# Kernel optimization log

Hardware: AMD Instinct MI355X
Metric: run time of the kernel (lower is better)

The kernel has to match this reference:

```python
import jax, jax.numpy as jnp
import numpy as np

B, N, EMB = 64, 2048, 128
K1 = 3
L = EMB - K1 + 1            # 126, width after conv1/conv2
K2 = L // 2 + 1             # 64, conv3 kernel width -> conv3 out width = K2 - 1 = 63


def _conv_relu(x, w, b):
    # x: [M, 1, H, W]; w: [O, 1, kh, kw]; VALID conv + bias + relu
    y = jax.lax.conv_general_dilated(
        x, w, window_strides=(1, 1), padding='VALID',
        dimension_numbers=('NCHW', 'OIHW', 'NCHW'))
    return jax.nn.relu(y + b[None, :, None, None])


def _score(pairs, W1, b1, W2, b2, W3, b3, fw1, fb1, fw2, fb2, fw3, fb3):
    # pairs: [M, 2, D] -> score [M]
    x = pairs[:, None]                                  # [M,1,2,D]
    c1 = _conv_relu(x, W1, b1)                          # [M,1,2,L]
    c2 = _conv_relu(x, W2, b2)                          # [M,1,1,L]
    c = jnp.concatenate([c1, c2], axis=2)               # [M,1,3,L]
    c3 = _conv_relu(c, W3, b3)                          # [M,1,1,K2-1]
    h = c3.reshape(c3.shape[0], -1)                     # [M,K2-1]
    h = h @ fw1.T + fb1                                 # [M,K2//4]
    h = h @ fw2.T + fb2                                 # [M,16]
    h = h @ fw3.T + fb3                                 # [M,1]
    return h[:, 0]


def setup_inputs() -> dict:
    key = jax.random.key(0)
    ks = jax.random.split(key, 12)
    users = jax.random.normal(ks[0], (B, N, EMB), jnp.float32)
    top_user = jax.random.normal(ks[1], (B, EMB), jnp.float32)
    question = jax.random.normal(ks[2], (B, EMB), jnp.float32)
    # ragged valid-lengths: uids nonzero for first `len` entries, zero after
    lengths = jax.random.randint(ks[3], (B,), 1, N + 1)
    vals = jax.random.randint(ks[4], (B, N), 1, 10000)
    uids = jnp.where(jnp.arange(N)[None, :] < lengths[:, None], vals, 0).astype(jnp.int64)
    s = 0.1
    return {
        'users': users, 'top_user': top_user, 'question': question, 'uids': uids,
        'W1': jax.random.normal(ks[5], (1, 1, 1, K1), jnp.float32) * s,
        'b1': jnp.zeros((1,), jnp.float32),
        'W2': jax.random.normal(ks[6], (1, 1, 2, K1), jnp.float32) * s,
        'b2': jnp.zeros((1,), jnp.float32),
        'W3': jax.random.normal(ks[7], (1, 1, 3, K2), jnp.float32) * s,
        'b3': jnp.zeros((1,), jnp.float32),
        'fw1': jax.random.normal(ks[8], (K2 // 4, K2 - 1), jnp.float32) * s,
        'fb1': jnp.zeros((K2 // 4,), jnp.float32),
        'fw2': jax.random.normal(ks[9], (16, K2 // 4), jnp.float32) * s,
        'fb2': jnp.zeros((16,), jnp.float32),
        'fw3': jax.random.normal(ks[10], (1, 16), jnp.float32) * s,
        'fb3': jnp.zeros((1,), jnp.float32),
    }


def reference(users, top_user, question, uids,
              W1, b1, W2, b2, W3, b3, fw1, fb1, fw2, fb2, fw3, fb3):
    b, n, d = users.shape
    params = (W1, b1, W2, b2, W3, b3, fw1, fb1, fw2, fb2, fw3, fb3)
    # low-rank pairs: (candidate user, question) for every candidate slot
    q = jnp.broadcast_to(question[:, None], (b, n, d))
    low = jnp.stack([users, q], axis=2).reshape(b * n, 2, d)      # [B*N,2,D]
    high = jnp.stack([top_user, question], axis=1)                # [B,2,D]
    low_s = _score(low, *params).reshape(b, n)                    # [B,N]
    high_s = _score(high, *params)                                # [B]
    # ragged length = index of first zero uid (torch loop breaks there)
    is_zero = uids == 0
    cnt = jnp.where(jnp.any(is_zero, axis=1), jnp.argmax(is_zero, axis=1), n)
    mask = (jnp.arange(n)[None, :] < cnt[:, None]).astype(low_s.dtype)
    return jnp.sum(jax.nn.sigmoid(low_s - high_s[:, None]) * mask)
```

## Files before the change

kernel.cpp:

```cpp
#include <hip/hip_runtime.h>
#include <hip/hip_bf16.h>

typedef __attribute__((ext_vector_type(8))) short short8v;
typedef __attribute__((ext_vector_type(4))) float float4v;

#define NB 64
#define NN 2048
#define ED 128
#define GRID_P 512

#define WS_WEFF  0
#define WS_BEFF  64
#define WS_SHIGH 128
#define WS_QTERM 192
#define WS_QPRE  (192+4096)
#define WS_BPACK (192+4096+8192)

static __device__ __forceinline__ unsigned int packbf2(float a, float b) {
    __hip_bfloat162 h = __float22bfloat162_rn(make_float2(a, b));
    return *(unsigned int*)&h;
}

__global__ __launch_bounds__(64) void k_prep(
    const float* __restrict__ top_user, const float* __restrict__ question,
    const float* __restrict__ W1, const float* __restrict__ b1,
    const float* __restrict__ W2, const float* __restrict__ b2,
    const float* __restrict__ W3, const float* __restrict__ b3,
    const float* __restrict__ fw1, const float* __restrict__ fb1,
    const float* __restrict__ fw2, const float* __restrict__ fb2,
    const float* __restrict__ fw3, const float* __restrict__ fb3,
    float* __restrict__ ws, float* __restrict__ out)
{
    const int lane = threadIdx.x;
    const int blk = blockIdx.x;
    __shared__ float g[16];
    __shared__ float w3s[192];
    w3s[lane] = W3[lane];
    w3s[64 + lane] = W3[64 + lane];
    w3s[128 + lane] = W3[128 + lane];
    if (lane < 16) {
        float s = 0.f;
        #pragma unroll
        for (int i = 0; i < 16; ++i) s += fw3[i] * fw2[i*16 + lane];
        g[lane] = s;
    }
    __syncthreads();

    if (blk >= NB) {
        const int kt = blk - NB;
        if (kt == 0) {
            if (lane == 0) out[0] = 0.f;
            float wv = 0.f;
            if (lane < 63) {
                #pragma unroll
                for (int k = 0; k < 16; ++k) wv += g[k] * fw1[k*63 + lane];
            }
            ws[WS_WEFF + lane] = wv;
            if (lane == 0) {
                float be = fb3[0];
                #pragma unroll
                for (int i = 0; i < 16; ++i) be += fw3[i] * fb2[i];
                #pragma unroll
                for (int k = 0; k < 16; ++k) be += g[k] * fb1[k];
                ws[WS_BEFF] = be;
            }
        }
        __hip_bfloat16* bp = (__hip_bfloat16*)(ws + WS_BPACK);
        const int g8 = (lane >> 4) * 8, li = lane & 15;
        #pragma unroll
        for (int nt = 0; nt < 4; ++nt) {
            const int tt = nt*16 + li;
            #pragma unroll
            for (int idx = 0; idx < 8; ++idx) {
                const int k = kt*32 + g8 + idx;
                const int j = k - tt;
                const int k2 = k - 128, j2 = k2 - tt;
                const bool v0 = (tt < 63) && (k < 126) && (j >= 0) && (j < 64);
                const bool v2 = (tt < 63) && (k2 >= 0) && (k2 < 126) && (j2 >= 0) && (j2 < 64);
                float v = (v0 ? w3s[j & 63] : 0.f) + (v2 ? w3s[128 + (j2 & 63)] : 0.f);
                bp[((kt*4 + nt)*64 + lane)*8 + idx] = __float2bfloat16(v);
            }
        }
        return;
    }

    float wv = 0.f;
    if (lane < 63) {
        #pragma unroll
        for (int k = 0; k < 16; ++k) wv += g[k] * fw1[k*63 + lane];
    }
    float be = fb3[0];
    #pragma unroll
    for (int i = 0; i < 16; ++i) be += fw3[i] * fb2[i];
    #pragma unroll
    for (int k = 0; k < 16; ++k) be += g[k] * fb1[k];

    __shared__ float q[132], tu[132], c1q[128], qt[64];
    __shared__ float4 D4[64];
    const int b = blk;
    ((float2*)q)[lane]  = ((const float2*)(question + b*ED))[lane];
    ((float2*)tu)[lane] = ((const float2*)(top_user + b*ED))[lane];
    if (lane == 63) {
        q[128]=0.f; q[129]=0.f; q[130]=0.f; q[131]=0.f;
        tu[128]=0.f; tu[129]=0.f; tu[130]=0.f; tu[131]=0.f;
    }
    __syncthreads();
    const float w10=W1[0], w11=W1[1], w12=W1[2];
    const float w20=W2[0], w21=W2[1], w22=W2[2];
    const float w23=W2[3], w24=W2[4], w25=W2[5];
    const float b1v=b1[0], b2v=b2[0], b3v=b3[0];
    const int i = 2*lane;
    float c1qa = fmaxf(b1v + w10*q[i]   + w11*q[i+1] + w12*q[i+2], 0.f);
    float c1qb = fmaxf(b1v + w10*q[i+1] + w11*q[i+2] + w12*q[i+3], 0.f);
    float qpa  = w23*q[i]   + w24*q[i+1] + w25*q[i+2];
    float qpb  = w23*q[i+1] + w24*q[i+2] + w25*q[i+3];
    float c1ta = fmaxf(b1v + w10*tu[i]   + w11*tu[i+1] + w12*tu[i+2], 0.f);
    float c1tb = fmaxf(b1v + w10*tu[i+1] + w11*tu[i+2] + w12*tu[i+3], 0.f);
    float c2a  = fmaxf(b2v + w20*tu[i]   + w21*tu[i+1] + w22*tu[i+2] + qpa, 0.f);
    float c2b  = fmaxf(b2v + w20*tu[i+1] + w21*tu[i+2] + w22*tu[i+3] + qpb, 0.f);
    if (lane == 63) { c1qa=0.f; c1qb=0.f; qpa=0.f; qpb=0.f; c1ta=0.f; c1tb=0.f; c2a=0.f; c2b=0.f; }
    c1q[i] = c1qa; c1q[i+1] = c1qb;
    ws[WS_QPRE + b*128 + i]     = qpa;
    ws[WS_QPRE + b*128 + i + 1] = qpb;
    D4[lane] = make_float4(c1ta, c2a, c1tb, c2b);
    __syncthreads();
    float qtv = 0.f;
    if (lane < 63) {
        #pragma unroll
        for (int j = 0; j < 64; ++j) qtv += w3s[64 + j] * c1q[lane + j];
    }
    qt[lane] = qtv;
    ws[WS_QTERM + b*64 + lane] = qtv + b3v;
    __syncthreads();
    float acc0 = b3v + qt[lane];
    float acc1 = 0.f;
    const float2* D2 = (const float2*)D4;
    #pragma unroll
    for (int j = 0; j < 64; ++j) {
        const float2 d = D2[lane + j];
        acc0 = fmaf(w3s[j],       d.x, acc0);
        acc1 = fmaf(w3s[128 + j], d.y, acc1);
    }
    float v = wv * fmaxf(acc0 + acc1, 0.f);
    #pragma unroll
    for (int off = 32; off > 0; off >>= 1) v += __shfl_xor(v, off, 64);
    if (lane == 0) ws[WS_SHIGH + b] = v + be;
}

__global__ __launch_bounds__(256) void k_pairs(
    const float* __restrict__ users, const int* __restrict__ uids,
    float* __restrict__ ws, float* __restrict__ out,
    const float* __restrict__ W1, const float* __restrict__ b1,
    const float* __restrict__ W2, const float* __restrict__ b2)
{
    __shared__ __align__(16) unsigned int X2[2][64][132];
    __shared__ float pscore[2][2][64];
    const int tid = threadIdx.x;
    const int w = tid >> 6, lane = tid & 63;
    const int bid = blockIdx.x;
    const int b = bid >> 3;
    const int cg = bid & 7;
    const int base = b*NN + cg*256;

    const int g = lane >> 4, li = lane & 15;
    const int nhalf = w >> 1;
    const int mbase = (w & 1) * 32;
    const int h = lane >> 5, j = lane & 31;
    const int r0 = w * 16;

    float4 bufA[8], bufB[8];
    #pragma unroll
    for (int pass = 0; pass < 8; ++pass) {
        const int r = r0 + pass*2 + h;
        bufA[pass] = *(const float4*)(users + (size_t)(base + r)*ED + 4*j);
    }
    const __hip_bfloat16* bp = (const __hip_bfloat16*)(ws + WS_BPACK);
    short8v bfr0[8], bfr1[8];
    #pragma unroll
    for (int kt = 0; kt < 8; ++kt) {
        bfr0[kt] = *(const short8v*)(bp + (((kt*4 + nhalf*2 + 0)*64 + lane) << 3));
        bfr1[kt] = *(const short8v*)(bp + (((kt*4 + nhalf*2 + 1)*64 + lane) << 3));
    }

    if (uids[base] == 0) return;
    const bool a1 = (uids[base +  64] != 0);
    const bool a2 = (uids[base + 128] != 0);
    const bool a3 = (uids[base + 192] != 0);

    const int m0 = (w == 0) ? uids[base + lane] : 1;
    const int m1 = (w == 0) ? uids[base +  64 + lane] : 1;
    const int m2 = (w == 0) ? uids[base + 128 + lane] : 1;
    const int m3 = (w == 0) ? uids[base + 192 + lane] : 1;

    #pragma unroll
    for (int pass = 0; pass < 8; ++pass) {
        const int r = r0 + pass*2 + h;
        bufB[pass] = *(const float4*)(users + (size_t)(base + 64 + r)*ED + 4*j);
    }

    const float w10=W1[0], w11=W1[1], w12=W1[2];
    const float w20=W2[0], w21=W2[1], w22=W2[2];
    const float b1v=b1[0], b2v=b2[0];

    const int t0 = nhalf*32 + li, t1 = t0 + 16;
    const float wf0 = ws[WS_WEFF + t0], wf1 = ws[WS_WEFF + t1];
    const float qt0 = ws[WS_QTERM + b*64 + t0], qt1 = ws[WS_QTERM + b*64 + t1];
    const float shigh = ws[WS_SHIGH + b], beff = ws[WS_BEFF];
    const float4 qp4 = *(const float4*)&ws[WS_QPRE + b*128 + 4*j];

#define PREP_BODY(BUF, XB)                                                          \
    {                                                                               \
        _Pragma("unroll")                                                           \
        for (int pass = 0; pass < 8; ++pass) {                                      \
            const int r = r0 + pass*2 + h;                                          \
            const float4 uu = BUF[pass];                                            \
            const float nx = __shfl(uu.x, (lane + 1) & 63, 64);                     \
            const float ny = __shfl(uu.y, (lane + 1) & 63, 64);                     \
            float c10 = fmaxf(b1v + w10*uu.x + w11*uu.y + w12*uu.z, 0.f);           \
            float c11 = fmaxf(b1v + w10*uu.y + w11*uu.z + w12*uu.w, 0.f);           \
            float c12 = fmaxf(b1v + w10*uu.z + w11*uu.w + w12*nx  , 0.f);           \
            float c13 = fmaxf(b1v + w10*uu.w + w11*nx   + w12*ny  , 0.f);           \
            float c20 = fmaxf(b2v + w20*uu.x + w21*uu.y + w22*uu.z + qp4.x, 0.f);   \
            float c21 = fmaxf(b2v + w20*uu.y + w21*uu.z + w22*uu.w + qp4.y, 0.f);   \
            float c22 = fmaxf(b2v + w20*uu.z + w21*uu.w + w22*nx   + qp4.z, 0.f);   \
            float c23 = fmaxf(b2v + w20*uu.w + w21*nx   + w22*ny   + qp4.w, 0.f);   \
            if (j == 31) { c12 = 0.f; c13 = 0.f; c22 = 0.f; c23 = 0.f; }            \
            uint2 v1; v1.x = packbf2(c10, c11); v1.y = packbf2(c12, c13);           \
            uint2 v2; v2.x = packbf2(c20, c21); v2.y = packbf2(c22, c23);           \
            *(uint2*)&X2[XB][r][2*j]      = v1;                                     \
            *(uint2*)&X2[XB][r][64 + 2*j] = v2;                                     \
        }                                                                           \
    }

    auto gemm = [&](int xb, int psl) {
        float4v acc00 = {0.f,0.f,0.f,0.f}, acc01 = {0.f,0.f,0.f,0.f};
        float4v acc10 = {0.f,0.f,0.f,0.f}, acc11 = {0.f,0.f,0.f,0.f};
        const char* Xb = (const char*)&X2[xb][0][0];
        #pragma unroll
        for (int kt = 0; kt < 8; ++kt) {
            const short8v aa0 = *(const short8v*)(Xb + (mbase + li)*528      + kt*64 + g*16);
            const short8v aa1 = *(const short8v*)(Xb + (mbase + 16 + li)*528 + kt*64 + g*16);
            acc00 = __builtin_amdgcn_mfma_f32_16x16x32_bf16(aa0, bfr0[kt], acc00, 0, 0, 0);
            acc01 = __builtin_amdgcn_mfma_f32_16x16x32_bf16(aa0, bfr1[kt], acc01, 0, 0, 0);
            acc10 = __builtin_amdgcn_mfma_f32_16x16x32_bf16(aa1, bfr0[kt], acc10, 0, 0, 0);
            acc11 = __builtin_amdgcn_mfma_f32_16x16x32_bf16(aa1, bfr1[kt], acc11, 0, 0, 0);
        }
        #pragma unroll
        for (int mi = 0; mi < 2; ++mi) {
            #pragma unroll
            for (int reg = 0; reg < 4; ++reg) {
                const float a0v = mi ? acc10[reg] : acc00[reg];
                const float a1v = mi ? acc11[reg] : acc01[reg];
                float v = wf0 * fmaxf(a0v + qt0, 0.f) + wf1 * fmaxf(a1v + qt1, 0.f);
                v += __shfl_xor(v, 1, 64);
                v += __shfl_xor(v, 2, 64);
                v += __shfl_xor(v, 4, 64);
                v += __shfl_xor(v, 8, 64);
                if (li == 0) pscore[psl][nhalf][mbase + mi*16 + g*4 + reg] = v;
            }
        }
    };

    float val = 0.f;
    auto sig = [&](int psl, int m) {
        if (w == 0) {
            const float d = pscore[psl][0][lane] + pscore[psl][1][lane] + beff - shigh;
            if (m != 0) val += 1.f / (1.f + __expf(-d));
        }
    };

    PREP_BODY(bufA, 0)
    __syncthreads();

    if (a2) {
        #pragma unroll
        for (int pass = 0; pass < 8; ++pass) {
            const int r = r0 + pass*2 + h;
            bufA[pass] = *(const float4*)(users + (size_t)(base + 128 + r)*ED + 4*j);
        }
    }
    gemm(0, 0);
    if (a1) PREP_BODY(bufB, 1)
    __syncthreads();

    sig(0, m0);
    if (a1) {
        if (a3) {
            #pragma unroll
            for (int pass = 0; pass < 8; ++pass) {
                const int r = r0 + pass*2 + h;
                bufB[pass] = *(const float4*)(users + (size_t)(base + 192 + r)*ED + 4*j);
            }
        }
        gemm(1, 1);
        if (a2) PREP_BODY(bufA, 0)
        __syncthreads();

        sig(1, m1);
        if (a2) {
            gemm(0, 0);
            if (a3) PREP_BODY(bufB, 1)
            __syncthreads();

            sig(0, m2);
            if (a3) {
                gemm(1, 1);
                __syncthreads();
                sig(1, m3);
            }
        }
    }

    if (w == 0) {
        #pragma unroll
        for (int off = 32; off > 0; off >>= 1) val += __shfl_xor(val, off, 64);
        if (lane == 0) atomicAdd(out, val);
    }
#undef PREP_BODY
}

extern "C" void kernel_launch(void* const* d_in, const int* in_sizes, int n_in,
                              void* d_out, int out_size, void* d_ws, size_t ws_size,
                              hipStream_t stream)
{
    const float* users    = (const float*)d_in[0];
    const float* top_user = (const float*)d_in[1];
    const float* question = (const float*)d_in[2];
    const int*   uids     = (const int*)d_in[3];
    const float* W1  = (const float*)d_in[4];
    const float* b1  = (const float*)d_in[5];
    const float* W2  = (const float*)d_in[6];
    const float* b2  = (const float*)d_in[7];
    const float* W3  = (const float*)d_in[8];
    const float* b3  = (const float*)d_in[9];
    const float* fw1 = (const float*)d_in[10];
    const float* fb1 = (const float*)d_in[11];
    const float* fw2 = (const float*)d_in[12];
    const float* fb2 = (const float*)d_in[13];
    const float* fw3 = (const float*)d_in[14];
    const float* fb3 = (const float*)d_in[15];
    float* ws  = (float*)d_ws;
    float* out = (float*)d_out;

    hipLaunchKernelGGL(k_prep, dim3(NB + 8), dim3(64), 0, stream,
                       top_user, question, W1, b1, W2, b2, W3, b3,
                       fw1, fb1, fw2, fb2, fw3, fb3, ws, out);
    hipLaunchKernelGGL(k_pairs, dim3(GRID_P), dim3(256), 0, stream,
                       users, uids, ws, out, W1, b1, W2, b2);
}
```

Before: 30.94 us.

## Restructure pair kernel into single-wave blocks of 64 rows without barriers

```diff
diff --git a/kernel.cpp b/kernel.cpp
--- a/kernel.cpp
+++ b/kernel.cpp
@@ -7,7 +7,7 @@
 #define NB 64
 #define NN 2048
 #define ED 128
-#define GRID_P 512
+#define GRID_P 2048
 
 #define WS_WEFF  0
 #define WS_BEFF  64
@@ -147,73 +147,66 @@
     if (lane == 0) ws[WS_SHIGH + b] = v + be;
 }
 
-__global__ __launch_bounds__(256) void k_pairs(
+__global__ __launch_bounds__(64, 2) void k_pairs(
     const float* __restrict__ users, const int* __restrict__ uids,
     float* __restrict__ ws, float* __restrict__ out,
     const float* __restrict__ W1, const float* __restrict__ b1,
     const float* __restrict__ W2, const float* __restrict__ b2)
 {
-    __shared__ __align__(16) unsigned int X2[2][64][132];
-    __shared__ float pscore[2][2][64];
-    const int tid = threadIdx.x;
-    const int w = tid >> 6, lane = tid & 63;
+    __shared__ __align__(16) unsigned int X[16][132];
+    const int lane = threadIdx.x;
     const int bid = blockIdx.x;
-    const int b = bid >> 3;
-    const int cg = bid & 7;
-    const int base = b*NN + cg*256;
+    const int b = bid >> 5;
+    const int cg = bid & 31;
+    const int base = b*NN + cg*64;
+
+    const int m_lane = uids[base + lane];
+    if (__shfl(m_lane, 0, 64) == 0) return;
+    const bool a1 = (__shfl(m_lane, 16, 64) != 0);
+    const bool a2 = (__shfl(m_lane, 32, 64) != 0);
+    const bool a3 = (__shfl(m_lane, 48, 64) != 0);
 
     const int g = lane >> 4, li = lane & 15;
-    const int nhalf = w >> 1;
-    const int mbase = (w & 1) * 32;
     const int h = lane >> 5, j = lane & 31;
-    const int r0 = w * 16;
-
-    float4 bufA[8], bufB[8];
+
+    float4 bufA[8];
     #pragma unroll
     for (int pass = 0; pass < 8; ++pass) {
-        const int r = r0 + pass*2 + h;
+        const int r = pass*2 + h;
         bufA[pass] = *(const float4*)(users + (size_t)(base + r)*ED + 4*j);
     }
+
     const __hip_bfloat16* bp = (const __hip_bfloat16*)(ws + WS_BPACK);
-    short8v bfr0[8], bfr1[8];
-    #pragma unroll
-    for (int kt = 0; kt < 8; ++kt) {
-        bfr0[kt] = *(const short8v*)(bp + (((kt*4 + nhalf*2 + 0)*64 + lane) << 3));
-        bfr1[kt] = *(const short8v*)(bp + (((kt*4 + nhalf*2 + 1)*64 + lane) << 3));
-    }
-
-    if (uids[base] == 0) return;
-    const bool a1 = (uids[base +  64] != 0);
-    const bool a2 = (uids[base + 128] != 0);
-    const bool a3 = (uids[base + 192] != 0);
-
-    const int m0 = (w == 0) ? uids[base + lane] : 1;
-    const int m1 = (w == 0) ? uids[base +  64 + lane] : 1;
-    const int m2 = (w == 0) ? uids[base + 128 + lane] : 1;
-    const int m3 = (w == 0) ? uids[base + 192 + lane] : 1;
-
-    #pragma unroll
-    for (int pass = 0; pass < 8; ++pass) {
-        const int r = r0 + pass*2 + h;
-        bufB[pass] = *(const float4*)(users + (size_t)(base + 64 + r)*ED + 4*j);
-    }
+    short8v bfr[32];
+    #pragma unroll
+    for (int nt = 0; nt < 4; ++nt) {
+        #pragma unroll
+        for (int kt = 0; kt < 8; ++kt) {
+            bfr[nt*8 + kt] = *(const short8v*)(bp + (((kt*4 + nt)*64 + lane) << 3));
+        }
+    }
+
+    float wfl[4], qtl[4];
+    #pragma unroll
+    for (int nt = 0; nt < 4; ++nt) {
+        wfl[nt] = ws[WS_WEFF + nt*16 + li];
+        qtl[nt] = ws[WS_QTERM + b*64 + nt*16 + li];
+    }
+    const float shigh = ws[WS_SHIGH + b], beff = ws[WS_BEFF];
+    const float4 qp4 = *(const float4*)&ws[WS_QPRE + b*128 + 4*j];
 
     const float w10=W1[0], w11=W1[1], w12=W1[2];
     const float w20=W2[0], w21=W2[1], w22=W2[2];
     const float b1v=b1[0], b2v=b2[0];
 
-    const int t0 = nhalf*32 + li, t1 = t0 + 16;
-    const float wf0 = ws[WS_WEFF + t0], wf1 = ws[WS_WEFF + t1];
-    const float qt0 = ws[WS_QTERM + b*64 + t0], qt1 = ws[WS_QTERM + b*64 + t1];
-    const float shigh = ws[WS_SHIGH + b], beff = ws[WS_BEFF];
-    const float4 qp4 = *(const float4*)&ws[WS_QPRE + b*128 + 4*j];
-
-#define PREP_BODY(BUF, XB)                                                          \
+    float val = 0.f;
+
+#define PREP_C()                                                                    \
     {                                                                               \
         _Pragma("unroll")                                                           \
         for (int pass = 0; pass < 8; ++pass) {                                      \
-            const int r = r0 + pass*2 + h;                                          \
-            const float4 uu = BUF[pass];                                            \
+            const int r = pass*2 + h;                                               \
+            const float4 uu = bufA[pass];                                           \
             const float nx = __shfl(uu.x, (lane + 1) & 63, 64);                     \
             const float ny = __shfl(uu.y, (lane + 1) & 63, 64);                     \
             float c10 = fmaxf(b1v + w10*uu.x + w11*uu.y + w12*uu.z, 0.f);           \
@@ -227,96 +220,76 @@
             if (j == 31) { c12 = 0.f; c13 = 0.f; c22 = 0.f; c23 = 0.f; }            \
             uint2 v1; v1.x = packbf2(c10, c11); v1.y = packbf2(c12, c13);           \
             uint2 v2; v2.x = packbf2(c20, c21); v2.y = packbf2(c22, c23);           \
-            *(uint2*)&X2[XB][r][2*j]      = v1;                                     \
-            *(uint2*)&X2[XB][r][64 + 2*j] = v2;                                     \
+            *(uint2*)&X[r][2*j]      = v1;                                          \
+            *(uint2*)&X[r][64 + 2*j] = v2;                                          \
         }                                                                           \
     }
 
-    auto gemm = [&](int xb, int psl) {
-        float4v acc00 = {0.f,0.f,0.f,0.f}, acc01 = {0.f,0.f,0.f,0.f};
-        float4v acc10 = {0.f,0.f,0.f,0.f}, acc11 = {0.f,0.f,0.f,0.f};
-        const char* Xb = (const char*)&X2[xb][0][0];
-        #pragma unroll
-        for (int kt = 0; kt < 8; ++kt) {
-            const short8v aa0 = *(const short8v*)(Xb + (mbase + li)*528      + kt*64 + g*16);
-            const short8v aa1 = *(const short8v*)(Xb + (mbase + 16 + li)*528 + kt*64 + g*16);
-            acc00 = __builtin_amdgcn_mfma_f32_16x16x32_bf16(aa0, bfr0[kt], acc00, 0, 0, 0);
-            acc01 = __builtin_amdgcn_mfma_f32_16x16x32_bf16(aa0, bfr1[kt], acc01, 0, 0, 0);
-            acc10 = __builtin_amdgcn_mfma_f32_16x16x32_bf16(aa1, bfr0[kt], acc10, 0, 0, 0);
-            acc11 = __builtin_amdgcn_mfma_f32_16x16x32_bf16(aa1, bfr1[kt], acc11, 0, 0, 0);
-        }
-        #pragma unroll
-        for (int mi = 0; mi < 2; ++mi) {
-            #pragma unroll
-            for (int reg = 0; reg < 4; ++reg) {
-                const float a0v = mi ? acc10[reg] : acc00[reg];
-                const float a1v = mi ? acc11[reg] : acc01[reg];
-                float v = wf0 * fmaxf(a0v + qt0, 0.f) + wf1 * fmaxf(a1v + qt1, 0.f);
-                v += __shfl_xor(v, 1, 64);
-                v += __shfl_xor(v, 2, 64);
-                v += __shfl_xor(v, 4, 64);
-                v += __shfl_xor(v, 8, 64);
-                if (li == 0) pscore[psl][nhalf][mbase + mi*16 + g*4 + reg] = v;
+#define LOAD_C(COFF)                                                                \
+    {                                                                               \
+        _Pragma("unroll")                                                           \
+        for (int pass = 0; pass < 8; ++pass) {                                      \
+            const int r = pass*2 + h;                                               \
+            bufA[pass] = *(const float4*)(users + (size_t)(base + (COFF) + r)*ED + 4*j); \
+        }                                                                           \
+    }
+
+#define GEMM_EP(COFF)                                                               \
+    {                                                                               \
+        float4v acc0 = {0.f,0.f,0.f,0.f}, acc1 = {0.f,0.f,0.f,0.f};                 \
+        float4v acc2 = {0.f,0.f,0.f,0.f}, acc3 = {0.f,0.f,0.f,0.f};                 \
+        const char* Xb = (const char*)&X[0][0];                                     \
+        _Pragma("unroll")                                                           \
+        for (int kt = 0; kt < 8; ++kt) {                                            \
+            const short8v a = *(const short8v*)(Xb + li*528 + kt*64 + g*16);        \
+            acc0 = __builtin_amdgcn_mfma_f32_16x16x32_bf16(a, bfr[0*8+kt], acc0, 0, 0, 0); \
+            acc1 = __builtin_amdgcn_mfma_f32_16x16x32_bf16(a, bfr[1*8+kt], acc1, 0, 0, 0); \
+            acc2 = __builtin_amdgcn_mfma_f32_16x16x32_bf16(a, bfr[2*8+kt], acc2, 0, 0, 0); \
+            acc3 = __builtin_amdgcn_mfma_f32_16x16x32_bf16(a, bfr[3*8+kt], acc3, 0, 0, 0); \
+        }                                                                           \
+        _Pragma("unroll")                                                           \
+        for (int reg = 0; reg < 4; ++reg) {                                         \
+            float v = wfl[0] * fmaxf(acc0[reg] + qtl[0], 0.f)                       \
+                    + wfl[1] * fmaxf(acc1[reg] + qtl[1], 0.f)                       \
+                    + wfl[2] * fmaxf(acc2[reg] + qtl[2], 0.f)                       \
+                    + wfl[3] * fmaxf(acc3[reg] + qtl[3], 0.f);                      \
+            v += __shfl_xor(v, 1, 64);                                              \
+            v += __shfl_xor(v, 2, 64);                                              \
+            v += __shfl_xor(v, 4, 64);                                              \
+            v += __shfl_xor(v, 8, 64);                                              \
+            const int mk = __shfl(m_lane, (COFF) + g*4 + reg, 64);                  \
+            if (li == 0 && mk != 0) {                                               \
+                const float d = v + beff - shigh;                                   \
+                val += 1.f / (1.f + __expf(-d));                                    \
+            }                                                                       \
+        }                                                                           \
+    }
+
+    PREP_C()
+    if (a1) LOAD_C(16)
+    GEMM_EP(0)
+    if (a1) {
+        PREP_C()
+        if (a2) LOAD_C(32)
+        GEMM_EP(16)
+        if (a2) {
+            PREP_C()
+            if (a3) LOAD_C(48)
+            GEMM_EP(32)
+            if (a3) {
+                PREP_C()
+                GEMM_EP(48)
             }
         }
-    };
-
-    float val = 0.f;
-    auto sig = [&](int psl, int m) {
-        if (w == 0) {
-            const float d = pscore[psl][0][lane] + pscore[psl][1][lane] + beff - shigh;
-            if (m != 0) val += 1.f / (1.f + __expf(-d));
-        }
-    };
-
-    PREP_BODY(bufA, 0)
-    __syncthreads();
-
-    if (a2) {
-        #pragma unroll
-        for (int pass = 0; pass < 8; ++pass) {
-            const int r = r0 + pass*2 + h;
-            bufA[pass] = *(const float4*)(users + (size_t)(base + 128 + r)*ED + 4*j);
-        }
-    }
-    gemm(0, 0);
-    if (a1) PREP_BODY(bufB, 1)
-    __syncthreads();
-
-    sig(0, m0);
-    if (a1) {
-        if (a3) {
-            #pragma unroll
-            for (int pass = 0; pass < 8; ++pass) {
-                const int r = r0 + pass*2 + h;
-                bufB[pass] = *(const float4*)(users + (size_t)(base + 192 + r)*ED + 4*j);
-            }
-        }
-        gemm(1, 1);
-        if (a2) PREP_BODY(bufA, 0)
-        __syncthreads();
-
-        sig(1, m1);
-        if (a2) {
-            gemm(0, 0);
-            if (a3) PREP_BODY(bufB, 1)
-            __syncthreads();
-
-            sig(0, m2);
-            if (a3) {
-                gemm(1, 1);
-                __syncthreads();
-                sig(1, m3);
-            }
-        }
-    }
-
-    if (w == 0) {
-        #pragma unroll
-        for (int off = 32; off > 0; off >>= 1) val += __shfl_xor(val, off, 64);
-        if (lane == 0) atomicAdd(out, val);
-    }
-#undef PREP_BODY
+    }
+
+    val += __shfl_xor(val, 16, 64);
+    val += __shfl_xor(val, 32, 64);
+    if (lane == 0) atomicAdd(out, val);
+
+#undef PREP_C
+#undef LOAD_C
+#undef GEMM_EP
 }
 
 extern "C" void kernel_launch(void* const* d_in, const int* in_sizes, int n_in,
@@ -345,6 +318,6 @@
     hipLaunchKernelGGL(k_prep, dim3(NB + 8), dim3(64), 0, stream,
                        top_user, question, W1, b1, W2, b2, W3, b3,
                        fw1, fb1, fw2, fb2, fw3, fb3, ws, out);
-    hipLaunchKernelGGL(k_pairs, dim3(GRID_P), dim3(256), 0, stream,
+    hipLaunchKernelGGL(k_pairs, dim3(GRID_P), dim3(64), 0, stream,
                        users, uids, ws, out, W1, b1, W2, b2);
 }
```

New measurement: 35.24 us. 1.14x slower.

## Compact active 64-row chunks into a work queue and load-balance across blocks

Applied to the files above, without the earlier changes.

```diff
diff --git a/kernel.cpp b/kernel.cpp
--- a/kernel.cpp
+++ b/kernel.cpp
@@ -15,6 +15,8 @@
 #define WS_QTERM 192
 #define WS_QPRE  (192+4096)
 #define WS_BPACK (192+4096+8192)
+#define WS_QCNT  (WS_BPACK+8192)
+#define WS_QLIST (WS_QCNT+8)
 
 static __device__ __forceinline__ unsigned int packbf2(float a, float b) {
     __hip_bfloat162 h = __float22bfloat162_rn(make_float2(a, b));
@@ -29,10 +31,30 @@
     const float* __restrict__ fw1, const float* __restrict__ fb1,
     const float* __restrict__ fw2, const float* __restrict__ fb2,
     const float* __restrict__ fw3, const float* __restrict__ fb3,
+    const int* __restrict__ uids,
     float* __restrict__ ws, float* __restrict__ out)
 {
     const int lane = threadIdx.x;
     const int blk = blockIdx.x;
+
+    if (blk >= NB + 8) {
+        const int s = blk - NB - 8;
+        int* qcnti  = (int*)(ws + WS_QCNT);
+        int* qlisti = (int*)(ws + WS_QLIST);
+        int running = 0;
+        #pragma unroll
+        for (int it = 0; it < 4; ++it) {
+            const int c = s*256 + it*64 + lane;
+            const int act = (uids[c * 64] != 0) ? 1 : 0;
+            const unsigned long long mask = __ballot(act);
+            const int pos = running + __popcll(mask & ((1ull << lane) - 1ull));
+            if (act) qlisti[s*256 + pos] = c;
+            running += (int)__popcll(mask);
+        }
+        if (lane == 0) qcnti[s] = running;
+        return;
+    }
+
     __shared__ float g[16];
     __shared__ float w3s[192];
     w3s[lane] = W3[lane];
@@ -158,22 +180,54 @@
     const int tid = threadIdx.x;
     const int w = tid >> 6, lane = tid & 63;
     const int bid = blockIdx.x;
-    const int b = bid >> 3;
-    const int cg = bid & 7;
-    const int base = b*NN + cg*256;
-
-    const int g = lane >> 4, li = lane & 15;
+
+    const int gfr = lane >> 4, li = lane & 15;
     const int nhalf = w >> 1;
     const int mbase = (w & 1) * 32;
     const int h = lane >> 5, j = lane & 31;
     const int r0 = w * 16;
 
+    const int* qcnti  = (const int*)(ws + WS_QCNT);
+    const int* qlisti = (const int*)(ws + WS_QLIST);
+    int pref[9]; pref[0] = 0;
+    #pragma unroll
+    for (int s = 0; s < 8; ++s) pref[s+1] = pref[s] + qcnti[s];
+    const int total = pref[8];
+    int myc[4];
+    #pragma unroll
+    for (int k = 0; k < 4; ++k) {
+        const int vid = bid + k*GRID_P;
+        int c = -1;
+        if (vid < total) {
+            int seg = 0;
+            #pragma unroll
+            for (int s = 1; s < 8; ++s) seg += (vid >= pref[s]) ? 1 : 0;
+            c = qlisti[seg*256 + (vid - pref[seg])];
+        }
+        myc[k] = c;
+    }
+    const int c0 = myc[0], c1 = myc[1], c2 = myc[2], c3 = myc[3];
+    if (c0 < 0) return;
+
+    const int pa0 = c0*64;
+    const int pa1 = (c1 >= 0) ? c1*64 : 0;
+    const int pa2 = (c2 >= 0) ? c2*64 : 0;
+    const int pa3 = (c3 >= 0) ? c3*64 : 0;
+
     float4 bufA[8], bufB[8];
     #pragma unroll
     for (int pass = 0; pass < 8; ++pass) {
         const int r = r0 + pass*2 + h;
-        bufA[pass] = *(const float4*)(users + (size_t)(base + r)*ED + 4*j);
-    }
+        bufA[pass] = *(const float4*)(users + (size_t)(pa0 + r)*ED + 4*j);
+    }
+    if (c1 >= 0) {
+        #pragma unroll
+        for (int pass = 0; pass < 8; ++pass) {
+            const int r = r0 + pass*2 + h;
+            bufB[pass] = *(const float4*)(users + (size_t)(pa1 + r)*ED + 4*j);
+        }
+    }
+
     const __hip_bfloat16* bp = (const __hip_bfloat16*)(ws + WS_BPACK);
     short8v bfr0[8], bfr1[8];
     #pragma unroll
@@ -182,33 +236,39 @@
         bfr1[kt] = *(const short8v*)(bp + (((kt*4 + nhalf*2 + 1)*64 + lane) << 3));
     }
 
-    if (uids[base] == 0) return;
-    const bool a1 = (uids[base +  64] != 0);
-    const bool a2 = (uids[base + 128] != 0);
-    const bool a3 = (uids[base + 192] != 0);
-
-    const int m0 = (w == 0) ? uids[base + lane] : 1;
-    const int m1 = (w == 0) ? uids[base +  64 + lane] : 1;
-    const int m2 = (w == 0) ? uids[base + 128 + lane] : 1;
-    const int m3 = (w == 0) ? uids[base + 192 + lane] : 1;
-
-    #pragma unroll
-    for (int pass = 0; pass < 8; ++pass) {
-        const int r = r0 + pass*2 + h;
-        bufB[pass] = *(const float4*)(users + (size_t)(base + 64 + r)*ED + 4*j);
-    }
+    const int t0 = nhalf*32 + li, t1 = t0 + 16;
+    const float wf0 = ws[WS_WEFF + t0], wf1 = ws[WS_WEFF + t1];
+    const float beff = ws[WS_BEFF];
+
+    const int b0 = c0 >> 5;
+    const float qta0 = ws[WS_QTERM + b0*64 + t0], qtb0 = ws[WS_QTERM + b0*64 + t1];
+    const float sh0 = ws[WS_SHIGH + b0];
+    const float4 qp0 = *(const float4*)&ws[WS_QPRE + b0*128 + 4*j];
+    const int m0 = (w == 0) ? uids[pa0 + lane] : 1;
+
+    const int b1i = (c1 >= 0) ? (c1 >> 5) : 0;
+    const float qta1 = ws[WS_QTERM + b1i*64 + t0], qtb1 = ws[WS_QTERM + b1i*64 + t1];
+    const float sh1 = ws[WS_SHIGH + b1i];
+    const float4 qp1 = *(const float4*)&ws[WS_QPRE + b1i*128 + 4*j];
+    const int m1 = (w == 0 && c1 >= 0) ? uids[pa1 + lane] : 1;
+
+    const int b2i = (c2 >= 0) ? (c2 >> 5) : 0;
+    const float qta2 = ws[WS_QTERM + b2i*64 + t0], qtb2 = ws[WS_QTERM + b2i*64 + t1];
+    const float sh2 = ws[WS_SHIGH + b2i];
+    const float4 qp2 = *(const float4*)&ws[WS_QPRE + b2i*128 + 4*j];
+    const int m2 = (w == 0 && c2 >= 0) ? uids[pa2 + lane] : 1;
+
+    const int b3i = (c3 >= 0) ? (c3 >> 5) : 0;
+    const float qta3 = ws[WS_QTERM + b3i*64 + t0], qtb3 = ws[WS_QTERM + b3i*64 + t1];
+    const float sh3 = ws[WS_SHIGH + b3i];
+    const float4 qp3 = *(const float4*)&ws[WS_QPRE + b3i*128 + 4*j];
+    const int m3 = (w == 0 && c3 >= 0) ? uids[pa3 + lane] : 1;
 
     const float w10=W1[0], w11=W1[1], w12=W1[2];
     const float w20=W2[0], w21=W2[1], w22=W2[2];
     const float b1v=b1[0], b2v=b2[0];
 
-    const int t0 = nhalf*32 + li, t1 = t0 + 16;
-    const float wf0 = ws[WS_WEFF + t0], wf1 = ws[WS_WEFF + t1];
-    const float qt0 = ws[WS_QTERM + b*64 + t0], qt1 = ws[WS_QTERM + b*64 + t1];
-    const float shigh = ws[WS_SHIGH + b], beff = ws[WS_BEFF];
-    const float4 qp4 = *(const float4*)&ws[WS_QPRE + b*128 + 4*j];
-
-#define PREP_BODY(BUF, XB)                                                          \
+#define PREP_BODY(BUF, XB, QP)                                                      \
     {                                                                               \
         _Pragma("unroll")                                                           \
         for (int pass = 0; pass < 8; ++pass) {                                      \
@@ -220,10 +280,10 @@
             float c11 = fmaxf(b1v + w10*uu.y + w11*uu.z + w12*uu.w, 0.f);           \
             float c12 = fmaxf(b1v + w10*uu.z + w11*uu.w + w12*nx  , 0.f);           \
             float c13 = fmaxf(b1v + w10*uu.w + w11*nx   + w12*ny  , 0.f);           \
-            float c20 = fmaxf(b2v + w20*uu.x + w21*uu.y + w22*uu.z + qp4.x, 0.f);   \
-            float c21 = fmaxf(b2v + w20*uu.y + w21*uu.z + w22*uu.w + qp4.y, 0.f);   \
-            float c22 = fmaxf(b2v + w20*uu.z + w21*uu.w + w22*nx   + qp4.z, 0.f);   \
-            float c23 = fmaxf(b2v + w20*uu.w + w21*nx   + w22*ny   + qp4.w, 0.f);   \
+            float c20 = fmaxf(b2v + w20*uu.x + w21*uu.y + w22*uu.z + QP.x, 0.f);    \
+            float c21 = fmaxf(b2v + w20*uu.y + w21*uu.z + w22*uu.w + QP.y, 0.f);    \
+            float c22 = fmaxf(b2v + w20*uu.z + w21*uu.w + w22*nx   + QP.z, 0.f);    \
+            float c23 = fmaxf(b2v + w20*uu.w + w21*nx   + w22*ny   + QP.w, 0.f);    \
             if (j == 31) { c12 = 0.f; c13 = 0.f; c22 = 0.f; c23 = 0.f; }            \
             uint2 v1; v1.x = packbf2(c10, c11); v1.y = packbf2(c12, c13);           \
             uint2 v2; v2.x = packbf2(c20, c21); v2.y = packbf2(c22, c23);           \
@@ -232,14 +292,23 @@
         }                                                                           \
     }
 
-    auto gemm = [&](int xb, int psl) {
+#define LOAD_INTO(BUF, PA)                                                          \
+    {                                                                               \
+        _Pragma("unroll")                                                           \
+        for (int pass = 0; pass < 8; ++pass) {                                      \
+            const int r = r0 + pass*2 + h;                                          \
+            BUF[pass] = *(const float4*)(users + (size_t)((PA) + r)*ED + 4*j);      \
+        }                                                                           \
+    }
+
+    auto gemm = [&](int xb, int psl, float qta, float qtb) {
         float4v acc00 = {0.f,0.f,0.f,0.f}, acc01 = {0.f,0.f,0.f,0.f};
         float4v acc10 = {0.f,0.f,0.f,0.f}, acc11 = {0.f,0.f,0.f,0.f};
         const char* Xb = (const char*)&X2[xb][0][0];
         #pragma unroll
         for (int kt = 0; kt < 8; ++kt) {
-            const short8v aa0 = *(const short8v*)(Xb + (mbase + li)*528      + kt*64 + g*16);
-            const short8v aa1 = *(const short8v*)(Xb + (mbase + 16 + li)*528 + kt*64 + g*16);
+            const short8v aa0 = *(const short8v*)(Xb + (mbase + li)*528      + kt*64 + gfr*16);
+            const short8v aa1 = *(const short8v*)(Xb + (mbase + 16 + li)*528 + kt*64 + gfr*16);
             acc00 = __builtin_amdgcn_mfma_f32_16x16x32_bf16(aa0, bfr0[kt], acc00, 0, 0, 0);
             acc01 = __builtin_amdgcn_mfma_f32_16x16x32_bf16(aa0, bfr1[kt], acc01, 0, 0, 0);
             acc10 = __builtin_amdgcn_mfma_f32_16x16x32_bf16(aa1, bfr0[kt], acc10, 0, 0, 0);
@@ -251,62 +320,50 @@
             for (int reg = 0; reg < 4; ++reg) {
                 const float a0v = mi ? acc10[reg] : acc00[reg];
                 const float a1v = mi ? acc11[reg] : acc01[reg];
-                float v = wf0 * fmaxf(a0v + qt0, 0.f) + wf1 * fmaxf(a1v + qt1, 0.f);
+                float v = wf0 * fmaxf(a0v + qta, 0.f) + wf1 * fmaxf(a1v + qtb, 0.f);
                 v += __shfl_xor(v, 1, 64);
                 v += __shfl_xor(v, 2, 64);
                 v += __shfl_xor(v, 4, 64);
                 v += __shfl_xor(v, 8, 64);
-                if (li == 0) pscore[psl][nhalf][mbase + mi*16 + g*4 + reg] = v;
+                if (li == 0) pscore[psl][nhalf][mbase + mi*16 + gfr*4 + reg] = v;
             }
         }
     };
 
     float val = 0.f;
-    auto sig = [&](int psl, int m) {
+    auto sig = [&](int psl, int m, float sh) {
         if (w == 0) {
-            const float d = pscore[psl][0][lane] + pscore[psl][1][lane] + beff - shigh;
+            const float d = pscore[psl][0][lane] + pscore[psl][1][lane] + beff - sh;
             if (m != 0) val += 1.f / (1.f + __expf(-d));
         }
     };
 
-    PREP_BODY(bufA, 0)
-    __syncthreads();
-
-    if (a2) {
-        #pragma unroll
-        for (int pass = 0; pass < 8; ++pass) {
-            const int r = r0 + pass*2 + h;
-            bufA[pass] = *(const float4*)(users + (size_t)(base + 128 + r)*ED + 4*j);
-        }
-    }
-    gemm(0, 0);
-    if (a1) PREP_BODY(bufB, 1)
-    __syncthreads();
-
-    sig(0, m0);
-    if (a1) {
-        if (a3) {
-            #pragma unroll
-            for (int pass = 0; pass < 8; ++pass) {
-                const int r = r0 + pass*2 + h;
-                bufB[pass] = *(const float4*)(users + (size_t)(base + 192 + r)*ED + 4*j);
-            }
-        }
-        gemm(1, 1);
-        if (a2) PREP_BODY(bufA, 0)
+    PREP_BODY(bufA, 0, qp0)
+    __syncthreads();
+
+    if (c2 >= 0) LOAD_INTO(bufA, pa2)
+    gemm(0, 0, qta0, qtb0);
+    if (c1 >= 0) PREP_BODY(bufB, 1, qp1)
+    __syncthreads();
+
+    sig(0, m0, sh0);
+    if (c1 >= 0) {
+        if (c3 >= 0) LOAD_INTO(bufB, pa3)
+        gemm(1, 1, qta1, qtb1);
+        if (c2 >= 0) PREP_BODY(bufA, 0, qp2)
         __syncthreads();
 
-        sig(1, m1);
-        if (a2) {
-            gemm(0, 0);
-            if (a3) PREP_BODY(bufB, 1)
+        sig(1, m1, sh1);
+        if (c2 >= 0) {
+            gemm(0, 0, qta2, qtb2);
+            if (c3 >= 0) PREP_BODY(bufB, 1, qp3)
             __syncthreads();
 
-            sig(0, m2);
-            if (a3) {
-                gemm(1, 1);
+            sig(0, m2, sh2);
+            if (c3 >= 0) {
+                gemm(1, 1, qta3, qtb3);
                 __syncthreads();
-                sig(1, m3);
+                sig(1, m3, sh3);
             }
         }
     }
@@ -317,6 +374,7 @@
         if (lane == 0) atomicAdd(out, val);
     }
 #undef PREP_BODY
+#undef LOAD_INTO
 }
 
 extern "C" void kernel_launch(void* const* d_in, const int* in_sizes, int n_in,
@@ -342,9 +400,9 @@
     float* ws  = (float*)d_ws;
     float* out = (float*)d_out;
 
-    hipLaunchKernelGGL(k_prep, dim3(NB + 8), dim3(64), 0, stream,
+    hipLaunchKernelGGL(k_prep, dim3(NB + 16), dim3(64), 0, stream,
                        top_user, question, W1, b1, W2, b2, W3, b3,
-                       fw1, fb1, fw2, fb2, fw3, fb3, ws, out);
+                       fw1, fb1, fw2, fb2, fw3, fb3, uids, ws, out);
     hipLaunchKernelGGL(k_pairs, dim3(GRID_P), dim3(256), 0, stream,
                        users, uids, ws, out, W1, b1, W2, b2);
 }
```

After: 28.08 us. 9.2% less time.
